# Kernel optimization log

Measured on AMD Instinct MI355X. Metric: run time of the kernel, lower is better.

## Reference

```python
import jax, jax.numpy as jnp
import numpy as np

N = 50000      # atoms
E = 1600000    # edges (avg degree 32)
G = 250        # crystals / graphs
H = 64         # hidden_channels
F = 64         # num_filters
NG = 50        # num_gaussians
NB = 3         # num_interactions
CUTOFF = 10.0


def setup_inputs() -> dict:
    key = jax.random.key(0)
    ks = jax.random.split(key, 20)
    s = 0.1
    z = jax.random.randint(ks[0], (N,), 0, 100, dtype=jnp.int32)
    pos = jax.random.uniform(ks[1], (N, 3), dtype=jnp.float32) * 5.0  # box keeps d < cutoff
    batch = jnp.sort(jax.random.randint(ks[2], (N,), 0, G, dtype=jnp.int32))
    edge_index = jax.random.randint(ks[3], (2, E), 0, N, dtype=jnp.int32)
    emb = jax.random.normal(ks[4], (100, H), dtype=jnp.float32)
    mlp_w1 = jax.random.normal(ks[5], (NB, NG, F), dtype=jnp.float32) * s
    mlp_b1 = jnp.zeros((NB, F), jnp.float32)
    mlp_w2 = jax.random.normal(ks[6], (NB, F, F), dtype=jnp.float32) * s
    mlp_b2 = jnp.zeros((NB, F), jnp.float32)
    cf1_w = jax.random.normal(ks[7], (NB, H, F), dtype=jnp.float32) * s  # lin1, no bias
    cf2_w = jax.random.normal(ks[8], (NB, F, H), dtype=jnp.float32) * s
    cf2_b = jnp.zeros((NB, H), jnp.float32)
    lin_w = jax.random.normal(ks[9], (NB, H, H), dtype=jnp.float32) * s
    lin_b = jnp.zeros((NB, H), jnp.float32)
    out1_w = jax.random.normal(ks[10], (H, H // 2), dtype=jnp.float32) * s
    out1_b = jnp.zeros((H // 2,), jnp.float32)
    out2_w = jax.random.normal(ks[11], (H // 2, 1), dtype=jnp.float32) * s
    out2_b = jnp.zeros((1,), jnp.float32)
    return dict(z=z, pos=pos, batch=batch, edge_index=edge_index, emb=emb,
                mlp_w1=mlp_w1, mlp_b1=mlp_b1, mlp_w2=mlp_w2, mlp_b2=mlp_b2,
                cf1_w=cf1_w, cf2_w=cf2_w, cf2_b=cf2_b, lin_w=lin_w, lin_b=lin_b,
                out1_w=out1_w, out1_b=out1_b, out2_w=out2_w, out2_b=out2_b)


def reference(z, pos, batch, edge_index, emb, mlp_w1, mlp_b1, mlp_w2, mlp_b2,
              cf1_w, cf2_w, cf2_b, lin_w, lin_b, out1_w, out1_b, out2_w, out2_b):
    ssp = lambda v: jax.nn.softplus(v) - jnp.log(2.0)  # shifted softplus
    src, dst = edge_index[0], edge_index[1]
    d = jnp.linalg.norm(pos[dst] - pos[src], axis=-1)          # [E]
    offset = jnp.linspace(0.0, CUTOFF, NG)
    coeff = -0.5 / (offset[1] - offset[0]) ** 2
    rbf = jnp.exp(coeff * (d[:, None] - offset) ** 2)          # [E, NG]
    C = 0.5 * (jnp.cos(d * jnp.pi / CUTOFF) + 1.0)             # cosine cutoff [E]
    h = emb[z]                                                 # [N, H]
    for t in range(NB):
        # CFConv filter network on edge RBF features
        Wf = (ssp(rbf @ mlp_w1[t] + mlp_b1[t]) @ mlp_w2[t] + mlp_b2[t]) * C[:, None]  # [E, F]
        msg = (h @ cf1_w[t])[src] * Wf                         # gather + modulate
        agg = jax.ops.segment_sum(msg, dst, num_segments=N)    # scatter-sum [N, F]
        x = ssp(agg @ cf2_w[t] + cf2_b[t]) @ lin_w[t] + lin_b[t]
        h = h + x                                              # residual
    g = jax.ops.segment_sum(h, batch, num_segments=G)          # per-graph readout [G, H]
    out = jax.nn.relu(g @ out1_w + out1_b) @ out2_w + out2_b   # head (dropout=eval identity)
    return out.squeeze(-1)                                     # [G]
```

## Files before the change

### kernel.cpp

```cpp
#include <hip/hip_runtime.h>
#include <math.h>

constexpr int NA = 50000;
constexpr int NE = 1600000;
constexpr int NGR = 250;
constexpr int HD = 64;
constexpr int NGAUSS = 50;
constexpr int NB = 3;
constexpr float FCUTOFF = 10.0f;

constexpr int NBINS = 8192;
constexpr float TBL_MAX = 8.6603f;
constexpr float TBL_STEP = TBL_MAX / NBINS;

constexpr int NBKT = (NA + 255) / 256;
constexpr int S1_EPB = 4096;
constexpr int S1_NB = (NE + S1_EPB - 1) / S1_EPB;

constexpr int NTILE = NA / 16;
constexpr int MM_NB = (NTILE + 3) / 4;
constexpr int NMAT = 15;
constexpr int WPREP_NB = NMAT * 4096 / 1024;
constexpr int TBL_NB = NB * (NBINS / 16) / 4;

typedef __attribute__((ext_vector_type(8))) short short8;
typedef __attribute__((ext_vector_type(4))) float floatx4;
typedef unsigned int uint;
typedef unsigned short ushort;

__device__ __forceinline__ float ssp(float v) {
    return fmaxf(v, 0.f) + log1pf(expf(-fabsf(v))) - 0.69314718055994530942f;
}
__device__ __forceinline__ ushort f2bf(float f) {
    uint u = __float_as_uint(f);
    return (ushort)((u + 0x7fffu + ((u >> 16) & 1u)) >> 16);
}
__device__ __forceinline__ float bf2f(ushort h) {
    return __uint_as_float(((uint)h) << 16);
}

__global__ __launch_bounds__(1024) void k_prepcount(const float* __restrict__ cf1w,
                                                    const float* __restrict__ cf2w,
                                                    const float* __restrict__ linw,
                                                    const float* __restrict__ mw1,
                                                    const float* __restrict__ mw2,
                                                    ushort* __restrict__ whi,
                                                    ushort* __restrict__ wlo,
                                                    const int* __restrict__ ei,
                                                    int* __restrict__ hist1) {
    __shared__ int lh[NBKT];
    if (blockIdx.x < WPREP_NB) {
        int idx = blockIdx.x * 1024 + threadIdx.x;
        int mi = idx >> 12;
        int rem = idx & 4095;
        int n = rem >> 6, k = rem & 63;
        float v;
        if (mi < 9) {
            int t = mi / 3, which = mi % 3;
            const float* src = (which == 0) ? cf1w : (which == 1) ? cf2w : linw;
            v = src[t * 4096 + k * 64 + n];
        } else if (mi < 12) {
            int t = mi - 9;
            v = (k < NGAUSS) ? mw1[(t * NGAUSS + k) * 64 + n] : 0.f;
        } else {
            int t = mi - 12;
            v = mw2[t * 4096 + k * 64 + n];
        }
        ushort hi = f2bf(v);
        ushort lo = f2bf(v - bf2f(hi));
        whi[mi * 4096 + n * 64 + k] = hi;
        wlo[mi * 4096 + n * 64 + k] = lo;
        return;
    }
    int cbid = blockIdx.x - WPREP_NB;
    for (int i = threadIdx.x; i < NBKT; i += 1024) lh[i] = 0;
    __syncthreads();
    int base = cbid * S1_EPB;
    #pragma unroll
    for (int i = 0; i < 4; i++) {
        int e = base + i * 1024 + threadIdx.x;
        if (e < NE) atomicAdd(&lh[ei[NE + e] >> 8], 1);
    }
    __syncthreads();
    for (int i = threadIdx.x; i < NBKT; i += 1024)
        if (lh[i]) atomicAdd(&hist1[i], lh[i]);
}

__global__ __launch_bounds__(256) void k_scan196(const int* __restrict__ hist1,
                                                 int* __restrict__ offsets1,
                                                 int* __restrict__ gcursor1,
                                                 int* __restrict__ offsets) {
    __shared__ int buf[256];
    int tid = threadIdx.x;
    int v = (tid < NBKT) ? hist1[tid] : 0;
    buf[tid] = v;
    __syncthreads();
    for (int off = 1; off < 256; off <<= 1) {
        int t = (tid >= off) ? buf[tid - off] : 0;
        __syncthreads();
        buf[tid] += t;
        __syncthreads();
    }
    int excl = buf[tid] - v;
    if (tid < NBKT) { offsets1[tid] = excl; gcursor1[tid] = excl; }
    if (tid == NBKT - 1) offsets1[NBKT] = excl + v;
    if (tid == 0) offsets[NA] = NE;
}

__global__ __launch_bounds__(1024) void k_sort1(const int* __restrict__ ei,
                                                const float* __restrict__ pos,
                                                int* __restrict__ gcursor1,
                                                int2* __restrict__ brec) {
    __shared__ int2 recs[S1_EPB];
    __shared__ unsigned char rbkt[S1_EPB];
    __shared__ int hist[NBKT];
    __shared__ int lcur[NBKT];
    __shared__ int delta[NBKT];
    __shared__ int scanbuf[256];
    int tid = threadIdx.x;
    for (int i = tid; i < NBKT; i += 1024) hist[i] = 0;
    __syncthreads();
    int2 myrec[4];
    int mybkt[4];
    int base = blockIdx.x * S1_EPB;
    #pragma unroll
    for (int i = 0; i < 4; i++) {
        int e = base + i * 1024 + tid;
        mybkt[i] = -1;
        if (e < NE) {
            int s = ei[e];
            int dt = ei[NE + e];
            float dx = pos[dt * 3 + 0] - pos[s * 3 + 0];
            float dy = pos[dt * 3 + 1] - pos[s * 3 + 1];
            float dz = pos[dt * 3 + 2] - pos[s * 3 + 2];
            float d = sqrtf(dx * dx + dy * dy + dz * dz);
            int bin = (int)(d * (1.0f / TBL_STEP) + 0.5f);
            bin = min(bin, NBINS - 1);
            myrec[i] = make_int2(s | ((dt & 255) << 17), bin);
            mybkt[i] = dt >> 8;
            atomicAdd(&hist[mybkt[i]], 1);
        }
    }
    __syncthreads();
    int v = (tid < NBKT) ? hist[tid] : 0;
    if (tid < 256) scanbuf[tid] = v;
    __syncthreads();
    for (int off = 1; off < 256; off <<= 1) {
        int t = (tid >= off && tid < 256) ? scanbuf[tid - off] : 0;
        __syncthreads();
        if (tid < 256) scanbuf[tid] += t;
        __syncthreads();
    }
    if (tid < NBKT) {
        int excl = scanbuf[tid] - v;
        lcur[tid] = excl;
        int gbase = atomicAdd(&gcursor1[tid], v);
        delta[tid] = gbase - excl;
    }
    __syncthreads();
    #pragma unroll
    for (int i = 0; i < 4; i++) {
        if (mybkt[i] >= 0) {
            int r = atomicAdd(&lcur[mybkt[i]], 1);
            recs[r] = myrec[i];
            rbkt[r] = (unsigned char)mybkt[i];
        }
    }
    __syncthreads();
    int total = min(S1_EPB, NE - base);
    for (int p = tid; p < total; p += 1024)
        brec[delta[rbkt[p]] + p] = recs[p];
}

__global__ __launch_bounds__(1024) void k_sort2(const int2* __restrict__ brec,
                                                const int* __restrict__ offsets1,
                                                uint* __restrict__ spayload,
                                                int* __restrict__ offsets) {
    __shared__ int cnt[256];
    __shared__ int lstart[256];
    __shared__ int lcur[256];
    int b = blockIdx.x;
    int tid = threadIdx.x;
    if (tid < 256) cnt[tid] = 0;
    __syncthreads();
    int rbase = offsets1[b], rend = offsets1[b + 1];
    for (int p = rbase + tid; p < rend; p += 1024)
        atomicAdd(&cnt[(brec[p].x >> 17) & 255], 1);
    __syncthreads();
    int v = (tid < 256) ? cnt[tid] : 0;
    if (tid < 256) lstart[tid] = v;
    __syncthreads();
    for (int off = 1; off < 256; off <<= 1) {
        int t = (tid >= off && tid < 256) ? lstart[tid - off] : 0;
        __syncthreads();
        if (tid < 256) lstart[tid] += t;
        __syncthreads();
    }
    if (tid < 256) {
        lstart[tid] -= v;
        lcur[tid] = rbase + lstart[tid];
        int node = (b << 8) + tid;
        if (node < NA) offsets[node] = rbase + lstart[tid];
    }
    __syncthreads();
    for (int p = rbase + tid; p < rend; p += 1024) {
        int2 r = brec[p];
        int slot = atomicAdd(&lcur[(r.x >> 17) & 255], 1);
        spayload[slot] = (uint)(r.x & 0xFFFF) | ((uint)r.y << 16);
    }
}

__device__ __forceinline__ void mk_frag2(float4 a0, float4 a1, short8& hi, short8& lo) {
    float av[8] = {a0.x, a0.y, a0.z, a0.w, a1.x, a1.y, a1.z, a1.w};
    #pragma unroll
    for (int j = 0; j < 8; j++) {
        ushort h = f2bf(av[j]);
        hi[j] = (short)h;
        lo[j] = (short)f2bf(av[j] - bf2f(h));
    }
}
__device__ __forceinline__ void mk_frag(const float* p, short8& hi, short8& lo) {
    mk_frag2(*(const float4*)p, *(const float4*)(p + 4), hi, lo);
}

__global__ __launch_bounds__(256) void k_tablehx0(const ushort* __restrict__ whi,
                                                  const ushort* __restrict__ wlo,
                                                  const float* __restrict__ b1,
                                                  const float* __restrict__ b2,
                                                  ushort* __restrict__ tblb,
                                                  const int* __restrict__ z,
                                                  const float* __restrict__ emb,
                                                  float* __restrict__ h,
                                                  ushort* __restrict__ hxb) {
    __shared__ ushort Thi[4][16][72];
    __shared__ ushort Tlo[4][16][72];
    int wave = threadIdx.x >> 6, lane = threadIdx.x & 63;
    int q = lane >> 4, ln = lane & 15;
    floatx4 acc[4];

    if (blockIdx.x < TBL_NB) {
        constexpr int TPB = NBINS / 16;
        int tile = blockIdx.x * 4 + wave;
        int t = tile / TPB;
        int bin0 = (tile % TPB) * 16;
        const float spacing = FCUTOFF / (NGAUSS - 1);
        const float coeff = -0.5f / (spacing * spacing);
        float d_ln = (bin0 + ln) * TBL_STEP;

        short8 ah[2], al[2];
        #pragma unroll
        for (int ks = 0; ks < 2; ks++) {
            #pragma unroll
            for (int j = 0; j < 8; j++) {
                int gg = ks * 32 + q * 8 + j;
                float u = d_ln - gg * spacing;
                float r = (gg < NGAUSS) ? expf(coeff * u * u) : 0.f;
                ushort hh = f2bf(r);
                ah[ks][j] = (short)hh;
                al[ks][j] = (short)f2bf(r - bf2f(hh));
            }
        }
        #pragma unroll
        for (int nt = 0; nt < 4; nt++) acc[nt] = (floatx4){0.f, 0.f, 0.f, 0.f};
        const ushort* w1h = whi + (9 + t) * 4096;
        const ushort* w1l = wlo + (9 + t) * 4096;
        #pragma unroll
        for (int ks = 0; ks < 2; ks++) {
            #pragma unroll
            for (int nt = 0; nt < 4; nt++) {
                int off = (nt * 16 + ln) * 64 + ks * 32 + q * 8;
                short8 bh = *(const short8*)(w1h + off);
                short8 bl = *(const short8*)(w1l + off);
                acc[nt] = __builtin_amdgcn_mfma_f32_16x16x32_bf16(ah[ks], bh, acc[nt], 0, 0, 0);
                acc[nt] = __builtin_amdgcn_mfma_f32_16x16x32_bf16(al[ks], bh, acc[nt], 0, 0, 0);
                acc[nt] = __builtin_amdgcn_mfma_f32_16x16x32_bf16(ah[ks], bl, acc[nt], 0, 0, 0);
            }
        }
        #pragma unroll
        for (int nt = 0; nt < 4; nt++) {
            float bias = b1[t * 64 + nt * 16 + ln];
            #pragma unroll
            for (int r = 0; r < 4; r++) {
                float v = ssp(acc[nt][r] + bias);
                ushort hi = f2bf(v);
                Thi[wave][q * 4 + r][nt * 16 + ln] = hi;
                Tlo[wave][q * 4 + r][nt * 16 + ln] = (ushort)f2bf(v - bf2f(hi));
            }
        }
        #pragma unroll
        for (int nt = 0; nt < 4; nt++) acc[nt] = (floatx4){0.f, 0.f, 0.f, 0.f};
        const ushort* w2h = whi + (12 + t) * 4096;
        const ushort* w2l = wlo + (12 + t) * 4096;
        #pragma unroll
        for (int ks = 0; ks < 2; ks++) {
            short8 ah2 = *(const short8*)&Thi[wave][ln][ks * 32 + q * 8];
            short8 al2 = *(const short8*)&Tlo[wave][ln][ks * 32 + q * 8];
            #pragma unroll
            for (int nt = 0; nt < 4; nt++) {
                int off = (nt * 16 + ln) * 64 + ks * 32 + q * 8;
                short8 bh = *(const short8*)(w2h + off);
                short8 bl = *(const short8*)(w2l + off);
                acc[nt] = __builtin_amdgcn_mfma_f32_16x16x32_bf16(ah2, bh, acc[nt], 0, 0, 0);
                acc[nt] = __builtin_amdgcn_mfma_f32_16x16x32_bf16(al2, bh, acc[nt], 0, 0, 0);
                acc[nt] = __builtin_amdgcn_mfma_f32_16x16x32_bf16(ah2, bl, acc[nt], 0, 0, 0);
            }
        }
        #pragma unroll
        for (int nt = 0; nt < 4; nt++) {
            float bias = b2[t * 64 + nt * 16 + ln];
            #pragma unroll
            for (int r = 0; r < 4; r++) {
                int bin = bin0 + q * 4 + r;
                float d = bin * TBL_STEP;
                float C = 0.5f * (cosf(d * (float)M_PI / FCUTOFF) + 1.0f);
                tblb[(size_t)(t * NBINS + bin) * 64 + nt * 16 + ln]
                    = f2bf((acc[nt][r] + bias) * C);
            }
        }
    } else {
        int tile = (blockIdx.x - TBL_NB) * 4 + wave;
        if (tile >= NTILE) return;
        int m0 = tile * 16;
        int row = m0 + ln;
        int zr = z[row];
        short8 ah[2], al[2];
        #pragma unroll
        for (int ks = 0; ks < 2; ks++) {
            float4 a0 = *(const float4*)(emb + zr * 64 + ks * 32 + q * 8);
            float4 a1 = *(const float4*)(emb + zr * 64 + ks * 32 + q * 8 + 4);
            *(float4*)(h + (size_t)row * 64 + ks * 32 + q * 8) = a0;
            *(float4*)(h + (size_t)row * 64 + ks * 32 + q * 8 + 4) = a1;
            mk_frag2(a0, a1, ah[ks], al[ks]);
        }
        #pragma unroll
        for (int nt = 0; nt < 4; nt++) acc[nt] = (floatx4){0.f, 0.f, 0.f, 0.f};
        #pragma unroll
        for (int ks = 0; ks < 2; ks++) {
            #pragma unroll
            for (int nt = 0; nt < 4; nt++) {
                int off = (nt * 16 + ln) * 64 + ks * 32 + q * 8;
                short8 bh = *(const short8*)(whi + off);
                short8 bl = *(const short8*)(wlo + off);
                acc[nt] = __builtin_amdgcn_mfma_f32_16x16x32_bf16(ah[ks], bh, acc[nt], 0, 0, 0);
                acc[nt] = __builtin_amdgcn_mfma_f32_16x16x32_bf16(al[ks], bh, acc[nt], 0, 0, 0);
                acc[nt] = __builtin_amdgcn_mfma_f32_16x16x32_bf16(ah[ks], bl, acc[nt], 0, 0, 0);
            }
        }
        #pragma unroll
        for (int nt = 0; nt < 4; nt++)
            #pragma unroll
            for (int r = 0; r < 4; r++)
                hxb[(size_t)(m0 + q * 4 + r) * 64 + nt * 16 + ln] = f2bf(acc[nt][r]);
    }
}

__global__ __launch_bounds__(256, 8) void k_interact(
        const uint* __restrict__ spayload, const int* __restrict__ offsets,
        const ushort* __restrict__ hx_in, const ushort* __restrict__ tbl_t,
        const ushort* __restrict__ whi, const ushort* __restrict__ wlo,
        int mi_cf2, int mi_lin, int mi_next,
        const float* __restrict__ cf2b_t, const float* __restrict__ linb_t,
        float* __restrict__ h, ushort* __restrict__ hx_out,
        const int* __restrict__ batch, float* __restrict__ g) {
    __shared__ __align__(16) float aggT[16][68];
    __shared__ ushort Thi[16][72];
    __shared__ ushort Tlo[16][72];
    __shared__ __align__(16) float Hst[16][68];
    int wave = threadIdx.x >> 6, lane = threadIdx.x & 63;
    int m0 = blockIdx.x * 16;

    {
        int e8 = lane >> 3, c8 = lane & 7;
        for (int i = 0; i < 4; i++) {
            int row = wave * 4 + i;
            int n = m0 + row;
            int start = offsets[n], end = offsets[n + 1];
            int nfull = (end - start) & ~7;
            int fend = start + nfull;
            float acc[8];
            #pragma unroll
            for (int j = 0; j < 8; j++) acc[j] = 0.f;
            #pragma unroll 2
            for (int base = start; base < fend; base += 8) {
                uint p = spayload[base + e8];
                int srcn = p & 0xFFFF;
                int b = p >> 16;
                uint4 wv = *(const uint4*)(tbl_t + ((size_t)b << 6) + (c8 << 3));
                uint4 hv = *(const uint4*)(hx_in + ((size_t)srcn << 6) + (c8 << 3));
                uint wa[4] = {wv.x, wv.y, wv.z, wv.w};
                uint ha[4] = {hv.x, hv.y, hv.z, hv.w};
                #pragma unroll
                for (int k = 0; k < 4; k++) {
                    float w0 = __uint_as_float(wa[k] << 16);
                    float w1 = __uint_as_float(wa[k] & 0xffff0000u);
                    float h0 = __uint_as_float(ha[k] << 16);
                    float h1 = __uint_as_float(ha[k] & 0xffff0000u);
                    acc[2 * k]     = fmaf(w0, h0, acc[2 * k]);
                    acc[2 * k + 1] = fmaf(w1, h1, acc[2 * k + 1]);
                }
            }
            if (fend + e8 < end) {
                uint p = spayload[fend + e8];
                int srcn = p & 0xFFFF;
                int b = p >> 16;
                uint4 wv = *(const uint4*)(tbl_t + ((size_t)b << 6) + (c8 << 3));
                uint4 hv = *(const uint4*)(hx_in + ((size_t)srcn << 6) + (c8 << 3));
                uint wa[4] = {wv.x, wv.y, wv.z, wv.w};
                uint ha[4] = {hv.x, hv.y, hv.z, hv.w};
                #pragma unroll
                for (int k = 0; k < 4; k++) {
                    float w0 = __uint_as_float(wa[k] << 16);
                    float w1 = __uint_as_float(wa[k] & 0xffff0000u);
                    float h0 = __uint_as_float(ha[k] << 16);
                    float h1 = __uint_as_float(ha[k] & 0xffff0000u);
                    acc[2 * k]     = fmaf(w0, h0, acc[2 * k]);
                    acc[2 * k + 1] = fmaf(w1, h1, acc[2 * k + 1]);
                }
            }
            #pragma unroll
            for (int j = 0; j < 8; j++) {
                acc[j] += __shfl_xor(acc[j], 8);
                acc[j] += __shfl_xor(acc[j], 16);
                acc[j] += __shfl_xor(acc[j], 32);
            }
            if (e8 == 0) {
                *(float4*)&aggT[row][c8 * 8] = make_float4(acc[0], acc[1], acc[2], acc[3]);
                *(float4*)&aggT[row][c8 * 8 + 4] = make_float4(acc[4], acc[5], acc[6], acc[7]);
            }
        }
    }
    __syncthreads();

    int q = lane >> 4, ln = lane & 15;
    floatx4 acc = (floatx4){0.f, 0.f, 0.f, 0.f};

    {
        short8 ah[2], al[2];
        #pragma unroll
        for (int ks = 0; ks < 2; ks++)
            mk_frag(&aggT[ln][ks * 32 + q * 8], ah[ks], al[ks]);
        const ushort* w2h = whi + mi_cf2 * 4096;
        const ushort* w2l = wlo + mi_cf2 * 4096;
        #pragma unroll
        for (int ks = 0; ks < 2; ks++) {
            int off = (wave * 16 + ln) * 64 + ks * 32 + q * 8;
            short8 bh = *(const short8*)(w2h + off);
            short8 bl = *(const short8*)(w2l + off);
            acc = __builtin_amdgcn_mfma_f32_16x16x32_bf16(ah[ks], bh, acc, 0, 0, 0);
            acc = __builtin_amdgcn_mfma_f32_16x16x32_bf16(al[ks], bh, acc, 0, 0, 0);
            acc = __builtin_amdgcn_mfma_f32_16x16x32_bf16(ah[ks], bl, acc, 0, 0, 0);
        }
        float bias = cf2b_t[wave * 16 + ln];
        #pragma unroll
        for (int r = 0; r < 4; r++) {
            float v = ssp(acc[r] + bias);
            ushort hi = f2bf(v);
            Thi[q * 4 + r][wave * 16 + ln] = hi;
            Tlo[q * 4 + r][wave * 16 + ln] = (ushort)f2bf(v - bf2f(hi));
        }
    }
    __syncthreads();

    {
        acc = (floatx4){0.f, 0.f, 0.f, 0.f};
        const ushort* wlh = whi + mi_lin * 4096;
        const ushort* wll = wlo + mi_lin * 4096;
        #pragma unroll
        for (int ks = 0; ks < 2; ks++) {
            short8 ah2 = *(const short8*)&Thi[ln][ks * 32 + q * 8];
            short8 al2 = *(const short8*)&Tlo[ln][ks * 32 + q * 8];
            int off = (wave * 16 + ln) * 64 + ks * 32 + q * 8;
            short8 bh = *(const short8*)(wlh + off);
            short8 bl = *(const short8*)(wll + off);
            acc = __builtin_amdgcn_mfma_f32_16x16x32_bf16(ah2, bh, acc, 0, 0, 0);
            acc = __builtin_amdgcn_mfma_f32_16x16x32_bf16(al2, bh, acc, 0, 0, 0);
            acc = __builtin_amdgcn_mfma_f32_16x16x32_bf16(ah2, bl, acc, 0, 0, 0);
        }
    }

    if (mi_next >= 0) {
        {
            float bias = linb_t[wave * 16 + ln];
            #pragma unroll
            for (int r = 0; r < 4; r++) {
                int idx = (m0 + q * 4 + r) * 64 + wave * 16 + ln;
                float hn = h[idx] + acc[r] + bias;
                h[idx] = hn;
                Hst[q * 4 + r][wave * 16 + ln] = hn;
            }
        }
        __syncthreads();
        {
            short8 ah3[2], al3[2];
            #pragma unroll
            for (int ks = 0; ks < 2; ks++)
                mk_frag(&Hst[ln][ks * 32 + q * 8], ah3[ks], al3[ks]);
            acc = (floatx4){0.f, 0.f, 0.f, 0.f};
            const ushort* wnh = whi + mi_next * 4096;
            const ushort* wnl = wlo + mi_next * 4096;
            #pragma unroll
            for (int ks = 0; ks < 2; ks++) {
                int off = (wave * 16 + ln) * 64 + ks * 32 + q * 8;
                short8 bh = *(const short8*)(wnh + off);
                short8 bl = *(const short8*)(wnl + off);
                acc = __builtin_amdgcn_mfma_f32_16x16x32_bf16(ah3[ks], bh, acc, 0, 0, 0);
                acc = __builtin_amdgcn_mfma_f32_16x16x32_bf16(al3[ks], bh, acc, 0, 0, 0);
                acc = __builtin_amdgcn_mfma_f32_16x16x32_bf16(ah3[ks], bl, acc, 0, 0, 0);
            }
            #pragma unroll
            for (int r = 0; r < 4; r++)
                hx_out[(size_t)(m0 + q * 4 + r) * 64 + wave * 16 + ln] = f2bf(acc[r]);
        }
    } else {
        int b0 = batch[m0], b15 = batch[m0 + 15];
        float bias = linb_t[wave * 16 + ln];
        if (b0 == b15) {
            float s = 4.0f * bias;
            #pragma unroll
            for (int r = 0; r < 4; r++) {
                int idx = (m0 + q * 4 + r) * 64 + wave * 16 + ln;
                s += h[idx] + acc[r];
            }
            s += __shfl_xor(s, 16);
            s += __shfl_xor(s, 32);
            if (q == 0) atomicAdd(&g[b0 * 64 + wave * 16 + ln], s);
        } else {
            #pragma unroll
            for (int r = 0; r < 4; r++) {
                int row = m0 + q * 4 + r;
                atomicAdd(&g[batch[row] * 64 + wave * 16 + ln],
                          h[row * 64 + wave * 16 + ln] + acc[r] + bias);
            }
        }
    }
}

__global__ __launch_bounds__(64) void k_head(const float* __restrict__ g,
                                             const float* __restrict__ o1w,
                                             const float* __restrict__ o1b,
                                             const float* __restrict__ o2w,
                                             const float* __restrict__ o2b,
                                             float* __restrict__ out) {
    int gi = blockIdx.x;
    int lane = threadIdx.x;
    float gv = g[gi * 64 + lane];
    float a = (lane < 32) ? o1b[lane] : 0.f;
    for (int k = 0; k < 64; k++) {
        float w = (lane < 32) ? o1w[k * 32 + lane] : 0.f;
        a = fmaf(__shfl(gv, k), w, a);
    }
    a = fmaxf(a, 0.f);
    float contrib = (lane < 32) ? a * o2w[lane] : 0.f;
    for (int off = 32; off > 0; off >>= 1) contrib += __shfl_down(contrib, off);
    if (lane == 0) out[gi] = contrib + o2b[0];
}

extern "C" void kernel_launch(void* const* d_in, const int* in_sizes, int n_in,
                              void* d_out, int out_size, void* d_ws, size_t ws_size,
                              hipStream_t stream) {
    (void)in_sizes; (void)n_in; (void)out_size; (void)ws_size;
    const int*   z    = (const int*)d_in[0];
    const float* pos  = (const float*)d_in[1];
    const int*   batch= (const int*)d_in[2];
    const int*   ei   = (const int*)d_in[3];
    const float* emb  = (const float*)d_in[4];
    const float* mw1  = (const float*)d_in[5];
    const float* mb1  = (const float*)d_in[6];
    const float* mw2  = (const float*)d_in[7];
    const float* mb2  = (const float*)d_in[8];
    const float* cf1w = (const float*)d_in[9];
    const float* cf2w = (const float*)d_in[10];
    const float* cf2b = (const float*)d_in[11];
    const float* linw = (const float*)d_in[12];
    const float* linb = (const float*)d_in[13];
    const float* o1w  = (const float*)d_in[14];
    const float* o1b  = (const float*)d_in[15];
    const float* o2w  = (const float*)d_in[16];
    const float* o2b  = (const float*)d_in[17];
    float* out = (float*)d_out;

    char* w = (char*)d_ws;
    auto take = [&](size_t bytes) {
        char* p = w;
        w += (bytes + 255) & ~size_t(255);
        return p;
    };
    int*    hist1    = (int*)take(NBKT * 4);
    int*    offsets1 = (int*)take((NBKT + 1) * 4);
    int*    gcursor1 = (int*)take(NBKT * 4);
    int*    offsets  = (int*)take((NA + 1) * 4);
    int2*   brec     = (int2*)take((size_t)NE * 8);
    uint*   spayload = (uint*)take((size_t)NE * 4);
    ushort* tblb     = (ushort*)take((size_t)NB * NBINS * HD * 2);
    ushort* whi      = (ushort*)take(NMAT * 4096 * 2);
    ushort* wlo      = (ushort*)take(NMAT * 4096 * 2);
    float*  h        = (float*)take((size_t)NA * HD * 4);
    ushort* hxA      = (ushort*)take((size_t)NA * HD * 2);
    ushort* hxB      = (ushort*)take((size_t)NA * HD * 2);
    float*  g        = (float*)take((size_t)NGR * HD * 4);

    hipMemsetAsync(hist1, 0, NBKT * 4, stream);
    hipMemsetAsync(g, 0, NGR * HD * 4, stream);

    k_prepcount<<<WPREP_NB + S1_NB, 1024, 0, stream>>>(cf1w, cf2w, linw, mw1, mw2,
                                                       whi, wlo, ei, hist1);
    k_scan196<<<1, 256, 0, stream>>>(hist1, offsets1, gcursor1, offsets);
    k_sort1<<<S1_NB, 1024, 0, stream>>>(ei, pos, gcursor1, brec);
    k_sort2<<<NBKT, 1024, 0, stream>>>(brec, offsets1, spayload, offsets);
    k_tablehx0<<<TBL_NB + MM_NB, 256, 0, stream>>>(whi, wlo, mb1, mb2, tblb,
                                                   z, emb, h, hxA);

    for (int t = 0; t < NB; t++) {
        const ushort* hin = (t == 1) ? hxB : hxA;
        ushort* hout = (t == 0) ? hxB : hxA;
        int mi_next = (t < NB - 1) ? ((t + 1) * 3 + 0) : -1;
        k_interact<<<NTILE, 256, 0, stream>>>(spayload, offsets, hin,
                                              tblb + (size_t)t * NBINS * HD,
                                              whi, wlo, t * 3 + 1, t * 3 + 2, mi_next,
                                              cf2b + t * 64, linb + t * 64,
                                              h, hout, batch, g);
    }
    k_head<<<NGR, 64, 0, stream>>>(g, o1w, o1b, o2w, o2b, out);
}
```

Baseline: 340.2 us.

## Fuse second sort pass into table/embedding kernel and shrink interact LDS

Merges the per-bucket second sort pass into the table-building and initial embedding kernel as extra 256-thread blocks, removing one kernel launch and letting independent work share the GPU. The sort blocks reuse the table kernel's shared memory for their counters. In the interaction kernel the Hst staging buffer now aliases aggT, with an added barrier, which lowers LDS use per block. The edge-gather loop unroll factor rises from 2 to 4. Sort blocks now run with 256 instead of 1024 threads, so each bucket is processed with less parallelism.

```diff
diff --git a/kernel.cpp b/kernel.cpp
--- a/kernel.cpp
+++ b/kernel.cpp
@@ -172,44 +172,6 @@
         brec[delta[rbkt[p]] + p] = recs[p];
 }
 
-__global__ __launch_bounds__(1024) void k_sort2(const int2* __restrict__ brec,
-                                                const int* __restrict__ offsets1,
-                                                uint* __restrict__ spayload,
-                                                int* __restrict__ offsets) {
-    __shared__ int cnt[256];
-    __shared__ int lstart[256];
-    __shared__ int lcur[256];
-    int b = blockIdx.x;
-    int tid = threadIdx.x;
-    if (tid < 256) cnt[tid] = 0;
-    __syncthreads();
-    int rbase = offsets1[b], rend = offsets1[b + 1];
-    for (int p = rbase + tid; p < rend; p += 1024)
-        atomicAdd(&cnt[(brec[p].x >> 17) & 255], 1);
-    __syncthreads();
-    int v = (tid < 256) ? cnt[tid] : 0;
-    if (tid < 256) lstart[tid] = v;
-    __syncthreads();
-    for (int off = 1; off < 256; off <<= 1) {
-        int t = (tid >= off && tid < 256) ? lstart[tid - off] : 0;
-        __syncthreads();
-        if (tid < 256) lstart[tid] += t;
-        __syncthreads();
-    }
-    if (tid < 256) {
-        lstart[tid] -= v;
-        lcur[tid] = rbase + lstart[tid];
-        int node = (b << 8) + tid;
-        if (node < NA) offsets[node] = rbase + lstart[tid];
-    }
-    __syncthreads();
-    for (int p = rbase + tid; p < rend; p += 1024) {
-        int2 r = brec[p];
-        int slot = atomicAdd(&lcur[(r.x >> 17) & 255], 1);
-        spayload[slot] = (uint)(r.x & 0xFFFF) | ((uint)r.y << 16);
-    }
-}
-
 __device__ __forceinline__ void mk_frag2(float4 a0, float4 a1, short8& hi, short8& lo) {
     float av[8] = {a0.x, a0.y, a0.z, a0.w, a1.x, a1.y, a1.z, a1.w};
     #pragma unroll
@@ -223,7 +185,11 @@
     mk_frag2(*(const float4*)p, *(const float4*)(p + 4), hi, lo);
 }
 
-__global__ __launch_bounds__(256) void k_tablehx0(const ushort* __restrict__ whi,
+__global__ __launch_bounds__(256) void k_sort2tab(const int2* __restrict__ brec,
+                                                  const int* __restrict__ offsets1,
+                                                  uint* __restrict__ spayload,
+                                                  int* __restrict__ offsets,
+                                                  const ushort* __restrict__ whi,
                                                   const ushort* __restrict__ wlo,
                                                   const float* __restrict__ b1,
                                                   const float* __restrict__ b2,
@@ -234,13 +200,48 @@
                                                   ushort* __restrict__ hxb) {
     __shared__ ushort Thi[4][16][72];
     __shared__ ushort Tlo[4][16][72];
-    int wave = threadIdx.x >> 6, lane = threadIdx.x & 63;
+    int tid = threadIdx.x;
+
+    if (blockIdx.x < NBKT) {
+        int* cnt = (int*)&Thi[0][0][0];
+        int* lstart = cnt + 256;
+        int* lcur = lstart + 256;
+        int b = blockIdx.x;
+        cnt[tid] = 0;
+        __syncthreads();
+        int rbase = offsets1[b], rend = offsets1[b + 1];
+        for (int p = rbase + tid; p < rend; p += 256)
+            atomicAdd(&cnt[(brec[p].x >> 17) & 255], 1);
+        __syncthreads();
+        int v = cnt[tid];
+        lstart[tid] = v;
+        __syncthreads();
+        for (int off = 1; off < 256; off <<= 1) {
+            int t = (tid >= off) ? lstart[tid - off] : 0;
+            __syncthreads();
+            lstart[tid] += t;
+            __syncthreads();
+        }
+        lstart[tid] -= v;
+        lcur[tid] = rbase + lstart[tid];
+        int node = (b << 8) + tid;
+        if (node < NA) offsets[node] = rbase + lstart[tid];
+        __syncthreads();
+        for (int p = rbase + tid; p < rend; p += 256) {
+            int2 r = brec[p];
+            int slot = atomicAdd(&lcur[(r.x >> 17) & 255], 1);
+            spayload[slot] = (uint)(r.x & 0xFFFF) | ((uint)r.y << 16);
+        }
+        return;
+    }
+
+    int wave = tid >> 6, lane = tid & 63;
     int q = lane >> 4, ln = lane & 15;
     floatx4 acc[4];
 
-    if (blockIdx.x < TBL_NB) {
+    if (blockIdx.x < NBKT + TBL_NB) {
         constexpr int TPB = NBINS / 16;
-        int tile = blockIdx.x * 4 + wave;
+        int tile = (blockIdx.x - NBKT) * 4 + wave;
         int t = tile / TPB;
         int bin0 = (tile % TPB) * 16;
         const float spacing = FCUTOFF / (NGAUSS - 1);
@@ -318,7 +319,7 @@
             }
         }
     } else {
-        int tile = (blockIdx.x - TBL_NB) * 4 + wave;
+        int tile = (blockIdx.x - NBKT - TBL_NB) * 4 + wave;
         if (tile >= NTILE) return;
         int m0 = tile * 16;
         int row = m0 + ln;
@@ -365,7 +366,7 @@
     __shared__ __align__(16) float aggT[16][68];
     __shared__ ushort Thi[16][72];
     __shared__ ushort Tlo[16][72];
-    __shared__ __align__(16) float Hst[16][68];
+    float (&Hst)[16][68] = aggT;
     int wave = threadIdx.x >> 6, lane = threadIdx.x & 63;
     int m0 = blockIdx.x * 16;
 
@@ -380,7 +381,7 @@
             float acc[8];
             #pragma unroll
             for (int j = 0; j < 8; j++) acc[j] = 0.f;
-            #pragma unroll 2
+            #pragma unroll 4
             for (int base = start; base < fend; base += 8) {
                 uint p = spayload[base + e8];
                 int srcn = p & 0xFFFF;
@@ -479,6 +480,7 @@
     }
 
     if (mi_next >= 0) {
+        __syncthreads();
         {
             float bias = linb_t[wave * 16 + ln];
             #pragma unroll
@@ -606,9 +608,9 @@
                                                        whi, wlo, ei, hist1);
     k_scan196<<<1, 256, 0, stream>>>(hist1, offsets1, gcursor1, offsets);
     k_sort1<<<S1_NB, 1024, 0, stream>>>(ei, pos, gcursor1, brec);
-    k_sort2<<<NBKT, 1024, 0, stream>>>(brec, offsets1, spayload, offsets);
-    k_tablehx0<<<TBL_NB + MM_NB, 256, 0, stream>>>(whi, wlo, mb1, mb2, tblb,
-                                                   z, emb, h, hxA);
+    k_sort2tab<<<NBKT + TBL_NB + MM_NB, 256, 0, stream>>>(brec, offsets1, spayload,
+                                                          offsets, whi, wlo, mb1, mb2,
+                                                          tblb, z, emb, h, hxA);
 
     for (int t = 0; t < NB; t++) {
         const ushort* hin = (t == 1) ? hxB : hxA;
```

New measurement: 362.3 us. +6.5%, slower.
